# Kernel tuning notes

Hardware: AMD Instinct MI355X
Metric: run time of the kernel (lower is better)

## Reference

```python
import jax, jax.numpy as jnp
import numpy as np

D_MODEL = 1024
N_HEADS = 16
HEAD_DIM = D_MODEL // N_HEADS


def setup_inputs() -> dict:
    key = jax.random.key(0)
    ks = jax.random.split(key, 9)
    B, S = 4, 2048
    x = jax.random.normal(ks[0], (B, S, D_MODEL), dtype=jnp.float32)
    # causal mask, broadcastable to (B, H, S, S); mask==0 -> -inf
    mask = jnp.tril(jnp.ones((S, S), dtype=jnp.int32))[None, None, :, :]
    s = 1.0 / np.sqrt(D_MODEL)
    wq = jax.random.normal(ks[1], (D_MODEL, D_MODEL), dtype=jnp.float32) * s
    wk = jax.random.normal(ks[2], (D_MODEL, D_MODEL), dtype=jnp.float32) * s
    wv = jax.random.normal(ks[3], (D_MODEL, D_MODEL), dtype=jnp.float32) * s
    wo = jax.random.normal(ks[4], (D_MODEL, D_MODEL), dtype=jnp.float32) * s
    bq = jnp.zeros((D_MODEL,), jnp.float32)
    bk = jnp.zeros((D_MODEL,), jnp.float32)
    bv = jnp.zeros((D_MODEL,), jnp.float32)
    bo = jnp.zeros((D_MODEL,), jnp.float32)
    return {"x": x, "mask": mask, "wq": wq, "bq": bq, "wk": wk, "bk": bk,
            "wv": wv, "bv": bv, "wo": wo, "bo": bo}


def reference(x, mask, wq, bq, wk, bk, wv, bv, wo, bo):
    B, S, D = x.shape
    H, Hd = N_HEADS, HEAD_DIM
    # torch nn.Linear: y = x @ W^T + b
    q = (jnp.einsum('bsd,ed->bse', x, wq) + bq).reshape(B, S, H, Hd).transpose(0, 2, 1, 3)
    k = (jnp.einsum('bsd,ed->bse', x, wk) + bk).reshape(B, S, H, Hd).transpose(0, 2, 1, 3)
    v = (jnp.einsum('bsd,ed->bse', x, wv) + bv).reshape(B, S, H, Hd).transpose(0, 2, 1, 3)
    scores = jnp.einsum('bhqd,bhkd->bhqk', q, k) / jnp.sqrt(jnp.float32(Hd))
    scores = jnp.where(mask == 0, -jnp.inf, scores)
    attn = jax.nn.softmax(scores, axis=-1)
    out = jnp.einsum('bhqk,bhkd->bhqd', attn, v)  # (B,H,S,Hd)
    out = out.transpose(0, 2, 1, 3).reshape(B, S, D)
    return jnp.einsum('bsd,ed->bse', out, wo) + bo
```

## Files before the change

kernel.cpp:

```cpp
#include <hip/hip_runtime.h>
#include <hip/hip_bf16.h>
#include <math.h>

using bf16x8 = __attribute__((ext_vector_type(8))) __bf16;
using bf16x4 = __attribute__((ext_vector_type(4))) __bf16;
using f32x4  = __attribute__((ext_vector_type(4))) float;
using f32x16 = __attribute__((ext_vector_type(16))) float;
using u32x4  = __attribute__((ext_vector_type(4))) unsigned;

static constexpr int S_ = 2048;
static constexpr float SCALE_L2E = 0.125f * 1.44269504088896340736f;

__device__ __forceinline__ void gload16(const void* g, void* lds) {
    __builtin_amdgcn_global_load_lds((const __attribute__((address_space(1))) void*)g,
                                     (__attribute__((address_space(3))) void*)lds, 16, 0, 0);
}

__device__ __forceinline__ unsigned pk2(float a, float b) {
    unsigned short lo = __builtin_bit_cast(unsigned short, (__bf16)a);
    unsigned short hi = __builtin_bit_cast(unsigned short, (__bf16)b);
    return (unsigned)lo | ((unsigned)hi << 16);
}

__global__ void cast_f32_bf16(const float* __restrict__ src, __bf16* __restrict__ dst, int n4) {
    int i = blockIdx.x * blockDim.x + threadIdx.x;
    if (i < n4) {
        float4 v = reinterpret_cast<const float4*>(src)[i];
        bf16x4 o = { (__bf16)v.x, (__bf16)v.y, (__bf16)v.z, (__bf16)v.w };
        reinterpret_cast<bf16x4*>(dst)[i] = o;
    }
}

template <int EPI>
__global__ __launch_bounds__(256) void gemm_bt(
    const __bf16* __restrict__ A, const __bf16* __restrict__ Bt,
    const float* __restrict__ b0, const float* __restrict__ b1, const float* __restrict__ b2,
    __bf16* __restrict__ Qo, __bf16* __restrict__ Ko, __bf16* __restrict__ Vo,
    float* __restrict__ Fo, int K) {
    __shared__ __align__(16) __bf16 LDS_[3][2][4096];
    const int t = threadIdx.x, l = t & 63, w = t >> 6;
    const int m0 = blockIdx.y * 128, n0 = blockIdx.x * 128;
    const int wm = (w >> 1) * 64, wn = (w & 1) * 64;
    f32x4 acc[4][4] = {};

    const int row0 = t >> 2, cw0 = t & 3;
    const int gc = cw0 ^ ((row0 >> 1) & 3);
    const __bf16* Ag0 = A + (size_t)(m0 + row0) * K + gc * 8;
    const __bf16* Ag1 = A + (size_t)(m0 + row0 + 64) * K + gc * 8;
    const __bf16* Bg0 = Bt + (size_t)(n0 + row0) * K + gc * 8;
    const __bf16* Bg1 = Bt + (size_t)(n0 + row0 + 64) * K + gc * 8;
    const int wo512 = w * 512;

#define STAGE(buf, k0)                                          \
    do {                                                        \
        gload16(Ag0 + (k0), &LDS_[buf][0][wo512]);              \
        gload16(Ag1 + (k0), &LDS_[buf][0][2048 + wo512]);       \
        gload16(Bg0 + (k0), &LDS_[buf][1][wo512]);              \
        gload16(Bg1 + (k0), &LDS_[buf][1][2048 + wo512]);       \
    } while (0)

    const int nk = K >> 5;
    STAGE(0, 0);
    STAGE(1, 32);
    int rb = 0, sb = 2;
    const int sc = (l >> 4) ^ ((l >> 1) & 3);
    for (int ki = 0; ki < nk; ++ki) {
        if (ki + 2 < nk) {
            STAGE(sb, (ki + 2) << 5);
            asm volatile("s_waitcnt vmcnt(8)" ::: "memory");
        } else if (ki + 1 < nk) {
            asm volatile("s_waitcnt vmcnt(4)" ::: "memory");
        } else {
            asm volatile("s_waitcnt vmcnt(0)" ::: "memory");
        }
        __builtin_amdgcn_s_barrier();
        const char* rdA = (const char*)&LDS_[rb][0][0];
        const char* rdB = (const char*)&LDS_[rb][1][0];
        bf16x8 af[4], bf[4];
#pragma unroll
        for (int i = 0; i < 4; ++i)
            af[i] = *reinterpret_cast<const bf16x8*>(rdA + (wm + i * 16 + (l & 15)) * 64 + sc * 16);
#pragma unroll
        for (int j = 0; j < 4; ++j)
            bf[j] = *reinterpret_cast<const bf16x8*>(rdB + (wn + j * 16 + (l & 15)) * 64 + sc * 16);
#pragma unroll
        for (int i = 0; i < 4; ++i)
#pragma unroll
            for (int j = 0; j < 4; ++j)
                acc[i][j] = __builtin_amdgcn_mfma_f32_16x16x32_bf16(af[i], bf[j], acc[i][j], 0, 0, 0);
        __builtin_amdgcn_s_barrier();
        rb = (rb == 2) ? 0 : rb + 1;
        sb = (sb == 2) ? 0 : sb + 1;
    }
#undef STAGE

    if (EPI == 0) {
        const int cls = n0 >> 10;
        if (cls < 2) {
            const float* bias = (cls == 0) ? b0 : b1;
#pragma unroll
            for (int j = 0; j < 4; ++j) {
                const int e = n0 + wn + j * 16 + (l & 15);
                const int eh = e & 1023;
                const int h = eh >> 6, hd = eh & 63;
                const float bv = bias[eh];
#pragma unroll
                for (int i = 0; i < 4; ++i)
#pragma unroll
                    for (int r = 0; r < 4; ++r) {
                        const int m = m0 + wm + i * 16 + ((l >> 4) << 2) + r;
                        const int b = m >> 11, s = m & 2047;
                        float v = acc[i][j][r] + bv;
                        if (cls == 0) v *= SCALE_L2E;
                        __bf16* dst = (cls == 0) ? Qo : Ko;
                        dst[((size_t)(b * 16 + h) * 2048 + s) * 64 + hd] = (__bf16)v;
                    }
            }
        } else {
            char* Tr = (char*)&LDS_[0][0][0];
#pragma unroll
            for (int j = 0; j < 4; ++j) {
                const int el = wn + j * 16 + (l & 15);
                const float bv = b2[(n0 & 1023) + el];
#pragma unroll
                for (int i = 0; i < 4; ++i) {
                    const int m4 = wm + i * 16 + ((l >> 4) << 2);
                    const int pos0 = (m4 & 112) | ((m4 & 4) << 1) | ((m4 & 8) >> 1);
                    bf16x4 pkv = { (__bf16)(acc[i][j][0] + bv), (__bf16)(acc[i][j][1] + bv),
                                   (__bf16)(acc[i][j][2] + bv), (__bf16)(acc[i][j][3] + bv) };
                    const int byt = el * 256 + ((pos0 * 2) ^ ((el & 7) << 4));
                    *reinterpret_cast<bf16x4*>(Tr + byt) = pkv;
                }
            }
            __syncthreads();
            const int b = m0 >> 11, sblk = m0 & 2047;
#pragma unroll
            for (int rr = 0; rr < 8; ++rr) {
                const int er = w * 32 + rr * 4 + (l >> 4);
                const int c = l & 15;
                const int slot = c ^ (er & 7);
                bf16x8 vv = *reinterpret_cast<const bf16x8*>(Tr + er * 256 + slot * 16);
                const int eg = (n0 & 1023) + er;
                const int h = eg >> 6, hd = eg & 63;
                char* dst = (char*)(Vo + ((size_t)(b * 16 + h) * 64 + hd) * 2048 + sblk) + c * 16;
                *reinterpret_cast<bf16x8*>(dst) = vv;
            }
        }
    } else {
#pragma unroll
        for (int j = 0; j < 4; ++j) {
            const int e = n0 + wn + j * 16 + (l & 15);
            const float bv = b0[e];
#pragma unroll
            for (int i = 0; i < 4; ++i)
#pragma unroll
                for (int r = 0; r < 4; ++r) {
                    const int m = m0 + wm + i * 16 + ((l >> 4) << 2) + r;
                    Fo[(size_t)m * 1024 + e] = acc[i][j][r] + bv;
                }
        }
    }
}

__global__ __launch_bounds__(256, 2) void attn_fwd(
    const __bf16* __restrict__ Qb, const __bf16* __restrict__ Kb,
    const __bf16* __restrict__ VTb, __bf16* __restrict__ Ob) {
    __shared__ __align__(16) __bf16 Ks[2][64 * 64];
    __shared__ __align__(16) __bf16 Vs[2][64 * 64];
    const int t = threadIdx.x, l = t & 63, w = t >> 6;
    const int id = blockIdx.x;
    const int bh = (id & 7) * 8 + ((id >> 3) & 7);
    const int xp = id >> 6;
    const int b = bh >> 4, hh = bh & 15;
    const int hl = l >> 5, l31 = l & 31;

    const __bf16* Qg = Qb + (size_t)bh * S_ * 64;
    const __bf16* Kg = Kb + (size_t)bh * S_ * 64;
    const __bf16* Vg = VTb + (size_t)bh * 64 * S_;

    const int l3 = l >> 3, gc8 = ((l & 7) ^ l3) * 8;
    const __bf16* Ksrc0 = Kg + (size_t)(16 * w + l3) * 64 + gc8;
    const __bf16* Ksrc1 = Kg + (size_t)(16 * w + 8 + l3) * 64 + gc8;
    const __bf16* Vsrc0 = Vg + (size_t)(16 * w + l3) * S_ + gc8;
    const __bf16* Vsrc1 = Vg + (size_t)(16 * w + 8 + l3) * S_ + gc8;
    __bf16* K0a = &Ks[0][w * 1024]; __bf16* K0b = K0a + 512;
    __bf16* K1a = &Ks[1][w * 1024]; __bf16* K1b = K1a + 512;
    __bf16* V0a = &Vs[0][w * 1024]; __bf16* V0b = V0a + 512;
    __bf16* V1a = &Vs[1][w * 1024]; __bf16* V1b = V1a + 512;

#pragma unroll 1
    for (int sidx = 0; sidx < 2; ++sidx) {
        const int qt = (sidx == 0) ? (15 - xp) : xp;
        const int qs = qt * 128 + w * 32;
        const int qg = qs + l31;

        bf16x8 qf[4];
#pragma unroll
        for (int c = 0; c < 4; ++c)
            qf[c] = *reinterpret_cast<const bf16x8*>(Qg + (size_t)qg * 64 + c * 16 + hl * 8);

        f32x16 o0 = {}, o1 = {};
        float m_r = -INFINITY, l_r = 0.f;

        const int ktmax = 2 * qt + 1;
        gload16(Ksrc0, K0a); gload16(Ksrc1, K0b);
        gload16(Vsrc0, V0a); gload16(Vsrc1, V0b);
        int cur = 0;
        for (int kt = 0; kt <= ktmax; ++kt) {
            if (kt < ktmax) {
                const size_t ko = (size_t)(kt + 1) * 4096;
                const int ho = (kt + 1) * 64;
                gload16(Ksrc0 + ko, (cur == 0) ? K1a : K0a);
                gload16(Ksrc1 + ko, (cur == 0) ? K1b : K0b);
                gload16(Vsrc0 + ho, (cur == 0) ? V1a : V0a);
                gload16(Vsrc1 + ho, (cur == 0) ? V1b : V0b);
                asm volatile("s_waitcnt vmcnt(4)" ::: "memory");
            } else {
                asm volatile("s_waitcnt vmcnt(0)" ::: "memory");
            }
            __builtin_amdgcn_s_barrier();
            const char* kb = (cur == 0) ? (const char*)Ks[0] : (const char*)Ks[1];
            const char* vb = (cur == 0) ? (const char*)Vs[0] : (const char*)Vs[1];
            if (kt * 64 <= qs + 31) {
                const int xs = (l & 7) << 4;
                f32x16 s0 = {}, s1 = {};
                __builtin_amdgcn_s_setprio(1);
#pragma unroll
                for (int c = 0; c < 4; ++c) {
                    bf16x8 kf0 = *reinterpret_cast<const bf16x8*>(kb + l31 * 128 + ((c * 32 + hl * 16) ^ xs));
                    s0 = __builtin_amdgcn_mfma_f32_32x32x16_bf16(kf0, qf[c], s0, 0, 0, 0);
                }
#pragma unroll
                for (int c = 0; c < 4; ++c) {
                    bf16x8 kf1 = *reinterpret_cast<const bf16x8*>(kb + (32 + l31) * 128 + ((c * 32 + hl * 16) ^ xs));
                    s1 = __builtin_amdgcn_mfma_f32_32x32x16_bf16(kf1, qf[c], s1, 0, 0, 0);
                }
                __builtin_amdgcn_s_setprio(0);
                float p0[16], p1[16];
                const int ktb = kt * 64;
                const bool bnd = (ktb + 63) > qs;
                if (bnd) {
#pragma unroll
                    for (int r = 0; r < 16; ++r) {
                        const int kvr = ktb + (r & 3) + 8 * (r >> 2) + 4 * hl;
                        p0[r] = (kvr > qg) ? -INFINITY : s0[r];
                        p1[r] = (kvr + 32 > qg) ? -INFINITY : s1[r];
                    }
                } else {
#pragma unroll
                    for (int r = 0; r < 16; ++r) { p0[r] = s0[r]; p1[r] = s1[r]; }
                }
                float mx[16];
#pragma unroll
                for (int r = 0; r < 16; ++r) mx[r] = fmaxf(p0[r], p1[r]);
#pragma unroll
                for (int s2 = 8; s2 > 0; s2 >>= 1)
#pragma unroll
                    for (int r = 0; r < 8; ++r) if (r < s2) mx[r] = fmaxf(mx[r], mx[r + s2]);
                float mt = fmaxf(mx[0], __shfl_xor(mx[0], 32));
                if (!__all(mt - m_r <= 8.0f)) {
                    const float mn = fmaxf(m_r, mt);
                    const float al = exp2f(m_r - mn);
                    m_r = mn;
                    l_r *= al;
#pragma unroll
                    for (int r = 0; r < 16; ++r) { o0[r] *= al; o1[r] *= al; }
                }
                float sm[16];
#pragma unroll
                for (int r = 0; r < 16; ++r) {
                    p0[r] = exp2f(p0[r] - m_r);
                    p1[r] = exp2f(p1[r] - m_r);
                    sm[r] = p0[r] + p1[r];
                }
#pragma unroll
                for (int s2 = 8; s2 > 0; s2 >>= 1)
#pragma unroll
                    for (int r = 0; r < 8; ++r) if (r < s2) sm[r] += sm[r + s2];
                l_r += sm[0] + __shfl_xor(sm[0], 32);
                u32x4 w0 = { pk2(p0[0], p0[1]), pk2(p0[2], p0[3]), pk2(p0[4], p0[5]), pk2(p0[6], p0[7]) };
                u32x4 w1 = { pk2(p0[8], p0[9]), pk2(p0[10], p0[11]), pk2(p0[12], p0[13]), pk2(p0[14], p0[15]) };
                u32x4 w2 = { pk2(p1[0], p1[1]), pk2(p1[2], p1[3]), pk2(p1[4], p1[5]), pk2(p1[6], p1[7]) };
                u32x4 w3 = { pk2(p1[8], p1[9]), pk2(p1[10], p1[11]), pk2(p1[12], p1[13]), pk2(p1[14], p1[15]) };
                bf16x8 pf0 = __builtin_bit_cast(bf16x8, w0);
                bf16x8 pf1 = __builtin_bit_cast(bf16x8, w1);
                bf16x8 pf2 = __builtin_bit_cast(bf16x8, w2);
                bf16x8 pf3 = __builtin_bit_cast(bf16x8, w3);
                __builtin_amdgcn_s_setprio(1);
#pragma unroll
                for (int a = 0; a < 2; ++a) {
                    const int rb2 = (a * 32 + l31) * 128;
                    bf16x8 vf0 = *reinterpret_cast<const bf16x8*>(vb + rb2 + ((0 * 32 + hl * 16) ^ xs));
                    bf16x8 vf1 = *reinterpret_cast<const bf16x8*>(vb + rb2 + ((1 * 32 + hl * 16) ^ xs));
                    bf16x8 vf2 = *reinterpret_cast<const bf16x8*>(vb + rb2 + ((2 * 32 + hl * 16) ^ xs));
                    bf16x8 vf3 = *reinterpret_cast<const bf16x8*>(vb + rb2 + ((3 * 32 + hl * 16) ^ xs));
                    if (a == 0) {
                        o0 = __builtin_amdgcn_mfma_f32_32x32x16_bf16(vf0, pf0, o0, 0, 0, 0);
                        o0 = __builtin_amdgcn_mfma_f32_32x32x16_bf16(vf1, pf1, o0, 0, 0, 0);
                        o0 = __builtin_amdgcn_mfma_f32_32x32x16_bf16(vf2, pf2, o0, 0, 0, 0);
                        o0 = __builtin_amdgcn_mfma_f32_32x32x16_bf16(vf3, pf3, o0, 0, 0, 0);
                    } else {
                        o1 = __builtin_amdgcn_mfma_f32_32x32x16_bf16(vf0, pf0, o1, 0, 0, 0);
                        o1 = __builtin_amdgcn_mfma_f32_32x32x16_bf16(vf1, pf1, o1, 0, 0, 0);
                        o1 = __builtin_amdgcn_mfma_f32_32x32x16_bf16(vf2, pf2, o1, 0, 0, 0);
                        o1 = __builtin_amdgcn_mfma_f32_32x32x16_bf16(vf3, pf3, o1, 0, 0, 0);
                    }
                }
                __builtin_amdgcn_s_setprio(0);
            }
            __builtin_amdgcn_s_barrier();
            cur ^= 1;
        }
        const float inv = 1.0f / l_r;
        __bf16* ob = Ob + (size_t)(b * 2048 + qg) * 1024 + hh * 64;
#pragma unroll
        for (int g = 0; g < 4; ++g) {
            bf16x4 v0 = { (__bf16)(o0[4 * g + 0] * inv), (__bf16)(o0[4 * g + 1] * inv),
                          (__bf16)(o0[4 * g + 2] * inv), (__bf16)(o0[4 * g + 3] * inv) };
            bf16x4 v1 = { (__bf16)(o1[4 * g + 0] * inv), (__bf16)(o1[4 * g + 1] * inv),
                          (__bf16)(o1[4 * g + 2] * inv), (__bf16)(o1[4 * g + 3] * inv) };
            *reinterpret_cast<bf16x4*>(ob + 8 * g + 4 * hl) = v0;
            *reinterpret_cast<bf16x4*>(ob + 32 + 8 * g + 4 * hl) = v1;
        }
    }
}

extern "C" void kernel_launch(void* const* d_in, const int* in_sizes, int n_in,
                              void* d_out, int out_size, void* d_ws, size_t ws_size,
                              hipStream_t stream) {
    const float* x  = (const float*)d_in[0];
    const float* wq = (const float*)d_in[2];
    const float* bq = (const float*)d_in[3];
    const float* wk = (const float*)d_in[4];
    const float* bk = (const float*)d_in[5];
    const float* wv = (const float*)d_in[6];
    const float* bv = (const float*)d_in[7];
    const float* wo = (const float*)d_in[8];
    const float* bo = (const float*)d_in[9];
    float* out = (float*)d_out;

    char* ws = (char*)d_ws;
    __bf16* xb   = (__bf16*)(ws);
    __bf16* wqkv = (__bf16*)(ws + 16777216);
    __bf16* wob  = (__bf16*)(ws + 23068672);
    __bf16* Qb   = (__bf16*)(ws + 25165824);
    __bf16* Kb   = (__bf16*)(ws + 41943040);
    __bf16* VTb  = (__bf16*)(ws + 58720256);
    __bf16* Ob   = (__bf16*)(ws + 75497472);

    cast_f32_bf16<<<8192, 256, 0, stream>>>(x, xb, 2097152);
    cast_f32_bf16<<<1024, 256, 0, stream>>>(wq, wqkv, 262144);
    cast_f32_bf16<<<1024, 256, 0, stream>>>(wk, wqkv + 1048576, 262144);
    cast_f32_bf16<<<1024, 256, 0, stream>>>(wv, wqkv + 2097152, 262144);
    cast_f32_bf16<<<1024, 256, 0, stream>>>(wo, wob, 262144);

    gemm_bt<0><<<dim3(24, 64), 256, 0, stream>>>(xb, wqkv, bq, bk, bv, Qb, Kb, VTb, nullptr, 1024);
    attn_fwd<<<512, 256, 0, stream>>>(Qb, Kb, VTb, Ob);
    gemm_bt<1><<<dim3(8, 64), 256, 0, stream>>>(Ob, wob, bo, nullptr, nullptr, nullptr, nullptr, nullptr, out, 1024);
}
```

Before: 188.0 us.

## Run heavy and light causal query tiles concurrently in one 8-wave block

The attention block now has 512 threads. Four waves handle the long causal query tile and four handle the paired short tile at the same time, instead of one 4-wave block doing the two tiles one after the other. Each K/V tile is loaded from global memory into LDS once and shared by both groups, which halves per-block K/V traffic and removes the serial second pass. The row-max reduction is also rewritten as a tree of 3-input maxes. The cost is that the short-tile waves sit idle at barriers for the rest of the loop. The __launch_bounds__(512,4) hint may also cap registers tightly enough to cause spills.

```diff
diff --git a/kernel.cpp b/kernel.cpp
--- a/kernel.cpp
+++ b/kernel.cpp
@@ -20,6 +20,10 @@
     unsigned short lo = __builtin_bit_cast(unsigned short, (__bf16)a);
     unsigned short hi = __builtin_bit_cast(unsigned short, (__bf16)b);
     return (unsigned)lo | ((unsigned)hi << 16);
+}
+
+__device__ __forceinline__ float max3f(float a, float b, float c) {
+    return fmaxf(fmaxf(a, b), c);
 }
 
 __global__ void cast_f32_bf16(const float* __restrict__ src, __bf16* __restrict__ dst, int n4) {
@@ -162,7 +166,7 @@
     }
 }
 
-__global__ __launch_bounds__(256, 2) void attn_fwd(
+__global__ __launch_bounds__(512, 4) void attn_fwd(
     const __bf16* __restrict__ Qb, const __bf16* __restrict__ Kb,
     const __bf16* __restrict__ VTb, __bf16* __restrict__ Ob) {
     __shared__ __align__(16) __bf16 Ks[2][64 * 64];
@@ -170,7 +174,8 @@
     const int t = threadIdx.x, l = t & 63, w = t >> 6;
     const int id = blockIdx.x;
     const int bh = (id & 7) * 8 + ((id >> 3) & 7);
-    const int xp = id >> 6;
+    const int g = id >> 6;
+    const int xp = (g < 4) ? g : 11 - g;
     const int b = bh >> 4, hh = bh & 15;
     const int hl = l >> 5, l31 = l & 31;
 
@@ -178,150 +183,143 @@
     const __bf16* Kg = Kb + (size_t)bh * S_ * 64;
     const __bf16* Vg = VTb + (size_t)bh * 64 * S_;
 
+    const int qt = (w >> 2) ? xp : (15 - xp);
+    const int sw = w & 3;
+    const int qs = qt * 128 + sw * 32;
+    const int qg = qs + l31;
+
     const int l3 = l >> 3, gc8 = ((l & 7) ^ l3) * 8;
-    const __bf16* Ksrc0 = Kg + (size_t)(16 * w + l3) * 64 + gc8;
-    const __bf16* Ksrc1 = Kg + (size_t)(16 * w + 8 + l3) * 64 + gc8;
-    const __bf16* Vsrc0 = Vg + (size_t)(16 * w + l3) * S_ + gc8;
-    const __bf16* Vsrc1 = Vg + (size_t)(16 * w + 8 + l3) * S_ + gc8;
-    __bf16* K0a = &Ks[0][w * 1024]; __bf16* K0b = K0a + 512;
-    __bf16* K1a = &Ks[1][w * 1024]; __bf16* K1b = K1a + 512;
-    __bf16* V0a = &Vs[0][w * 1024]; __bf16* V0b = V0a + 512;
-    __bf16* V1a = &Vs[1][w * 1024]; __bf16* V1b = V1a + 512;
-
-#pragma unroll 1
-    for (int sidx = 0; sidx < 2; ++sidx) {
-        const int qt = (sidx == 0) ? (15 - xp) : xp;
-        const int qs = qt * 128 + w * 32;
-        const int qg = qs + l31;
-
-        bf16x8 qf[4];
-#pragma unroll
-        for (int c = 0; c < 4; ++c)
-            qf[c] = *reinterpret_cast<const bf16x8*>(Qg + (size_t)qg * 64 + c * 16 + hl * 8);
-
-        f32x16 o0 = {}, o1 = {};
-        float m_r = -INFINITY, l_r = 0.f;
-
-        const int ktmax = 2 * qt + 1;
-        gload16(Ksrc0, K0a); gload16(Ksrc1, K0b);
-        gload16(Vsrc0, V0a); gload16(Vsrc1, V0b);
-        int cur = 0;
-        for (int kt = 0; kt <= ktmax; ++kt) {
-            if (kt < ktmax) {
-                const size_t ko = (size_t)(kt + 1) * 4096;
-                const int ho = (kt + 1) * 64;
-                gload16(Ksrc0 + ko, (cur == 0) ? K1a : K0a);
-                gload16(Ksrc1 + ko, (cur == 0) ? K1b : K0b);
-                gload16(Vsrc0 + ho, (cur == 0) ? V1a : V0a);
-                gload16(Vsrc1 + ho, (cur == 0) ? V1b : V0b);
-                asm volatile("s_waitcnt vmcnt(4)" ::: "memory");
+    const __bf16* Ksrc = Kg + (size_t)(8 * w + l3) * 64 + gc8;
+    const __bf16* Vsrc = Vg + (size_t)(8 * w + l3) * S_ + gc8;
+    __bf16* Kd0 = &Ks[0][w * 512]; __bf16* Kd1 = &Ks[1][w * 512];
+    __bf16* Vd0 = &Vs[0][w * 512]; __bf16* Vd1 = &Vs[1][w * 512];
+
+    bf16x8 qf[4];
+#pragma unroll
+    for (int c = 0; c < 4; ++c)
+        qf[c] = *reinterpret_cast<const bf16x8*>(Qg + (size_t)qg * 64 + c * 16 + hl * 8);
+
+    f32x16 o0 = {}, o1 = {};
+    float m_r = -INFINITY, l_r = 0.f;
+
+    const int ktmax_blk = 2 * (15 - xp) + 1;
+    gload16(Ksrc, Kd0);
+    gload16(Vsrc, Vd0);
+    int cur = 0;
+    for (int kt = 0; kt <= ktmax_blk; ++kt) {
+        if (kt < ktmax_blk) {
+            const size_t ko = (size_t)(kt + 1) * 4096;
+            gload16(Ksrc + ko, (cur == 0) ? Kd1 : Kd0);
+            gload16(Vsrc + (kt + 1) * 64, (cur == 0) ? Vd1 : Vd0);
+            asm volatile("s_waitcnt vmcnt(2)" ::: "memory");
+        } else {
+            asm volatile("s_waitcnt vmcnt(0)" ::: "memory");
+        }
+        __builtin_amdgcn_s_barrier();
+        const char* kb = (cur == 0) ? (const char*)Ks[0] : (const char*)Ks[1];
+        const char* vb = (cur == 0) ? (const char*)Vs[0] : (const char*)Vs[1];
+        if (kt * 64 <= qs + 31) {
+            const int xs = (l & 7) << 4;
+            f32x16 s0 = {}, s1 = {};
+            __builtin_amdgcn_s_setprio(1);
+#pragma unroll
+            for (int c = 0; c < 4; ++c) {
+                bf16x8 kf0 = *reinterpret_cast<const bf16x8*>(kb + l31 * 128 + ((c * 32 + hl * 16) ^ xs));
+                s0 = __builtin_amdgcn_mfma_f32_32x32x16_bf16(kf0, qf[c], s0, 0, 0, 0);
+            }
+#pragma unroll
+            for (int c = 0; c < 4; ++c) {
+                bf16x8 kf1 = *reinterpret_cast<const bf16x8*>(kb + (32 + l31) * 128 + ((c * 32 + hl * 16) ^ xs));
+                s1 = __builtin_amdgcn_mfma_f32_32x32x16_bf16(kf1, qf[c], s1, 0, 0, 0);
+            }
+            __builtin_amdgcn_s_setprio(0);
+            float p0[16], p1[16];
+            const int ktb = kt * 64;
+            const bool bnd = (ktb + 63) > qs;
+            if (bnd) {
+#pragma unroll
+                for (int r = 0; r < 16; ++r) {
+                    const int kvr = ktb + (r & 3) + 8 * (r >> 2) + 4 * hl;
+                    p0[r] = (kvr > qg) ? -INFINITY : s0[r];
+                    p1[r] = (kvr + 32 > qg) ? -INFINITY : s1[r];
+                }
             } else {
-                asm volatile("s_waitcnt vmcnt(0)" ::: "memory");
-            }
-            __builtin_amdgcn_s_barrier();
-            const char* kb = (cur == 0) ? (const char*)Ks[0] : (const char*)Ks[1];
-            const char* vb = (cur == 0) ? (const char*)Vs[0] : (const char*)Vs[1];
-            if (kt * 64 <= qs + 31) {
-                const int xs = (l & 7) << 4;
-                f32x16 s0 = {}, s1 = {};
-                __builtin_amdgcn_s_setprio(1);
-#pragma unroll
-                for (int c = 0; c < 4; ++c) {
-                    bf16x8 kf0 = *reinterpret_cast<const bf16x8*>(kb + l31 * 128 + ((c * 32 + hl * 16) ^ xs));
-                    s0 = __builtin_amdgcn_mfma_f32_32x32x16_bf16(kf0, qf[c], s0, 0, 0, 0);
+#pragma unroll
+                for (int r = 0; r < 16; ++r) { p0[r] = s0[r]; p1[r] = s1[r]; }
+            }
+            float mx[16];
+#pragma unroll
+            for (int r = 0; r < 16; ++r) mx[r] = fmaxf(p0[r], p1[r]);
+            float u0 = max3f(mx[0], mx[1], mx[2]);
+            float u1 = max3f(mx[3], mx[4], mx[5]);
+            float u2 = max3f(mx[6], mx[7], mx[8]);
+            float u3 = max3f(mx[9], mx[10], mx[11]);
+            float u4 = max3f(mx[12], mx[13], mx[14]);
+            float mt = fmaxf(max3f(u0, u1, u2), max3f(u3, u4, mx[15]));
+            mt = fmaxf(mt, __shfl_xor(mt, 32));
+            if (!__all(mt - m_r <= 8.0f)) {
+                const float mn = fmaxf(m_r, mt);
+                const float al = exp2f(m_r - mn);
+                m_r = mn;
+                l_r *= al;
+#pragma unroll
+                for (int r = 0; r < 16; ++r) { o0[r] *= al; o1[r] *= al; }
+            }
+            float sm[16];
+#pragma unroll
+            for (int r = 0; r < 16; ++r) {
+                p0[r] = exp2f(p0[r] - m_r);
+                p1[r] = exp2f(p1[r] - m_r);
+                sm[r] = p0[r] + p1[r];
+            }
+#pragma unroll
+            for (int s2 = 8; s2 > 0; s2 >>= 1)
+#pragma unroll
+                for (int r = 0; r < 8; ++r) if (r < s2) sm[r] += sm[r + s2];
+            l_r += sm[0] + __shfl_xor(sm[0], 32);
+            u32x4 w0 = { pk2(p0[0], p0[1]), pk2(p0[2], p0[3]), pk2(p0[4], p0[5]), pk2(p0[6], p0[7]) };
+            u32x4 w1 = { pk2(p0[8], p0[9]), pk2(p0[10], p0[11]), pk2(p0[12], p0[13]), pk2(p0[14], p0[15]) };
+            u32x4 w2 = { pk2(p1[0], p1[1]), pk2(p1[2], p1[3]), pk2(p1[4], p1[5]), pk2(p1[6], p1[7]) };
+            u32x4 w3 = { pk2(p1[8], p1[9]), pk2(p1[10], p1[11]), pk2(p1[12], p1[13]), pk2(p1[14], p1[15]) };
+            bf16x8 pf0 = __builtin_bit_cast(bf16x8, w0);
+            bf16x8 pf1 = __builtin_bit_cast(bf16x8, w1);
+            bf16x8 pf2 = __builtin_bit_cast(bf16x8, w2);
+            bf16x8 pf3 = __builtin_bit_cast(bf16x8, w3);
+            __builtin_amdgcn_s_setprio(1);
+#pragma unroll
+            for (int a = 0; a < 2; ++a) {
+                const int rb2 = (a * 32 + l31) * 128;
+                bf16x8 vf0 = *reinterpret_cast<const bf16x8*>(vb + rb2 + ((0 * 32 + hl * 16) ^ xs));
+                bf16x8 vf1 = *reinterpret_cast<const bf16x8*>(vb + rb2 + ((1 * 32 + hl * 16) ^ xs));
+                bf16x8 vf2 = *reinterpret_cast<const bf16x8*>(vb + rb2 + ((2 * 32 + hl * 16) ^ xs));
+                bf16x8 vf3 = *reinterpret_cast<const bf16x8*>(vb + rb2 + ((3 * 32 + hl * 16) ^ xs));
+                if (a == 0) {
+                    o0 = __builtin_amdgcn_mfma_f32_32x32x16_bf16(vf0, pf0, o0, 0, 0, 0);
+                    o0 = __builtin_amdgcn_mfma_f32_32x32x16_bf16(vf1, pf1, o0, 0, 0, 0);
+                    o0 = __builtin_amdgcn_mfma_f32_32x32x16_bf16(vf2, pf2, o0, 0, 0, 0);
+                    o0 = __builtin_amdgcn_mfma_f32_32x32x16_bf16(vf3, pf3, o0, 0, 0, 0);
+                } else {
+                    o1 = __builtin_amdgcn_mfma_f32_32x32x16_bf16(vf0, pf0, o1, 0, 0, 0);
+                    o1 = __builtin_amdgcn_mfma_f32_32x32x16_bf16(vf1, pf1, o1, 0, 0, 0);
+                    o1 = __builtin_amdgcn_mfma_f32_32x32x16_bf16(vf2, pf2, o1, 0, 0, 0);
+                    o1 = __builtin_amdgcn_mfma_f32_32x32x16_bf16(vf3, pf3, o1, 0, 0, 0);
                 }
-#pragma unroll
-                for (int c = 0; c < 4; ++c) {
-                    bf16x8 kf1 = *reinterpret_cast<const bf16x8*>(kb + (32 + l31) * 128 + ((c * 32 + hl * 16) ^ xs));
-                    s1 = __builtin_amdgcn_mfma_f32_32x32x16_bf16(kf1, qf[c], s1, 0, 0, 0);
-                }
-                __builtin_amdgcn_s_setprio(0);
-                float p0[16], p1[16];
-                const int ktb = kt * 64;
-                const bool bnd = (ktb + 63) > qs;
-                if (bnd) {
-#pragma unroll
-                    for (int r = 0; r < 16; ++r) {
-                        const int kvr = ktb + (r & 3) + 8 * (r >> 2) + 4 * hl;
-                        p0[r] = (kvr > qg) ? -INFINITY : s0[r];
-                        p1[r] = (kvr + 32 > qg) ? -INFINITY : s1[r];
-                    }
-                } else {
-#pragma unroll
-                    for (int r = 0; r < 16; ++r) { p0[r] = s0[r]; p1[r] = s1[r]; }
-                }
-                float mx[16];
-#pragma unroll
-                for (int r = 0; r < 16; ++r) mx[r] = fmaxf(p0[r], p1[r]);
-#pragma unroll
-                for (int s2 = 8; s2 > 0; s2 >>= 1)
-#pragma unroll
-                    for (int r = 0; r < 8; ++r) if (r < s2) mx[r] = fmaxf(mx[r], mx[r + s2]);
-                float mt = fmaxf(mx[0], __shfl_xor(mx[0], 32));
-                if (!__all(mt - m_r <= 8.0f)) {
-                    const float mn = fmaxf(m_r, mt);
-                    const float al = exp2f(m_r - mn);
-                    m_r = mn;
-                    l_r *= al;
-#pragma unroll
-                    for (int r = 0; r < 16; ++r) { o0[r] *= al; o1[r] *= al; }
-                }
-                float sm[16];
-#pragma unroll
-                for (int r = 0; r < 16; ++r) {
-                    p0[r] = exp2f(p0[r] - m_r);
-                    p1[r] = exp2f(p1[r] - m_r);
-                    sm[r] = p0[r] + p1[r];
-                }
-#pragma unroll
-                for (int s2 = 8; s2 > 0; s2 >>= 1)
-#pragma unroll
-                    for (int r = 0; r < 8; ++r) if (r < s2) sm[r] += sm[r + s2];
-                l_r += sm[0] + __shfl_xor(sm[0], 32);
-                u32x4 w0 = { pk2(p0[0], p0[1]), pk2(p0[2], p0[3]), pk2(p0[4], p0[5]), pk2(p0[6], p0[7]) };
-                u32x4 w1 = { pk2(p0[8], p0[9]), pk2(p0[10], p0[11]), pk2(p0[12], p0[13]), pk2(p0[14], p0[15]) };
-                u32x4 w2 = { pk2(p1[0], p1[1]), pk2(p1[2], p1[3]), pk2(p1[4], p1[5]), pk2(p1[6], p1[7]) };
-                u32x4 w3 = { pk2(p1[8], p1[9]), pk2(p1[10], p1[11]), pk2(p1[12], p1[13]), pk2(p1[14], p1[15]) };
-                bf16x8 pf0 = __builtin_bit_cast(bf16x8, w0);
-                bf16x8 pf1 = __builtin_bit_cast(bf16x8, w1);
-                bf16x8 pf2 = __builtin_bit_cast(bf16x8, w2);
-                bf16x8 pf3 = __builtin_bit_cast(bf16x8, w3);
-                __builtin_amdgcn_s_setprio(1);
-#pragma unroll
-                for (int a = 0; a < 2; ++a) {
-                    const int rb2 = (a * 32 + l31) * 128;
-                    bf16x8 vf0 = *reinterpret_cast<const bf16x8*>(vb + rb2 + ((0 * 32 + hl * 16) ^ xs));
-                    bf16x8 vf1 = *reinterpret_cast<const bf16x8*>(vb + rb2 + ((1 * 32 + hl * 16) ^ xs));
-                    bf16x8 vf2 = *reinterpret_cast<const bf16x8*>(vb + rb2 + ((2 * 32 + hl * 16) ^ xs));
-                    bf16x8 vf3 = *reinterpret_cast<const bf16x8*>(vb + rb2 + ((3 * 32 + hl * 16) ^ xs));
-                    if (a == 0) {
-                        o0 = __builtin_amdgcn_mfma_f32_32x32x16_bf16(vf0, pf0, o0, 0, 0, 0);
-                        o0 = __builtin_amdgcn_mfma_f32_32x32x16_bf16(vf1, pf1, o0, 0, 0, 0);
-                        o0 = __builtin_amdgcn_mfma_f32_32x32x16_bf16(vf2, pf2, o0, 0, 0, 0);
-                        o0 = __builtin_amdgcn_mfma_f32_32x32x16_bf16(vf3, pf3, o0, 0, 0, 0);
-                    } else {
-                        o1 = __builtin_amdgcn_mfma_f32_32x32x16_bf16(vf0, pf0, o1, 0, 0, 0);
-                        o1 = __builtin_amdgcn_mfma_f32_32x32x16_bf16(vf1, pf1, o1, 0, 0, 0);
-                        o1 = __builtin_amdgcn_mfma_f32_32x32x16_bf16(vf2, pf2, o1, 0, 0, 0);
-                        o1 = __builtin_amdgcn_mfma_f32_32x32x16_bf16(vf3, pf3, o1, 0, 0, 0);
-                    }
-                }
-                __builtin_amdgcn_s_setprio(0);
-            }
-            __builtin_amdgcn_s_barrier();
-            cur ^= 1;
-        }
-        const float inv = 1.0f / l_r;
-        __bf16* ob = Ob + (size_t)(b * 2048 + qg) * 1024 + hh * 64;
-#pragma unroll
-        for (int g = 0; g < 4; ++g) {
-            bf16x4 v0 = { (__bf16)(o0[4 * g + 0] * inv), (__bf16)(o0[4 * g + 1] * inv),
-                          (__bf16)(o0[4 * g + 2] * inv), (__bf16)(o0[4 * g + 3] * inv) };
-            bf16x4 v1 = { (__bf16)(o1[4 * g + 0] * inv), (__bf16)(o1[4 * g + 1] * inv),
-                          (__bf16)(o1[4 * g + 2] * inv), (__bf16)(o1[4 * g + 3] * inv) };
-            *reinterpret_cast<bf16x4*>(ob + 8 * g + 4 * hl) = v0;
-            *reinterpret_cast<bf16x4*>(ob + 32 + 8 * g + 4 * hl) = v1;
-        }
+            }
+            __builtin_amdgcn_s_setprio(0);
+        }
+        __builtin_amdgcn_s_barrier();
+        cur ^= 1;
+    }
+    const float inv = 1.0f / l_r;
+    __bf16* ob = Ob + (size_t)(b * 2048 + qg) * 1024 + hh * 64;
+#pragma unroll
+    for (int gq = 0; gq < 4; ++gq) {
+        bf16x4 v0 = { (__bf16)(o0[4 * gq + 0] * inv), (__bf16)(o0[4 * gq + 1] * inv),
+                      (__bf16)(o0[4 * gq + 2] * inv), (__bf16)(o0[4 * gq + 3] * inv) };
+        bf16x4 v1 = { (__bf16)(o1[4 * gq + 0] * inv), (__bf16)(o1[4 * gq + 1] * inv),
+                      (__bf16)(o1[4 * gq + 2] * inv), (__bf16)(o1[4 * gq + 3] * inv) };
+        *reinterpret_cast<bf16x4*>(ob + 8 * gq + 4 * hl) = v0;
+        *reinterpret_cast<bf16x4*>(ob + 32 + 8 * gq + 4 * hl) = v1;
     }
 }
 
@@ -355,6 +353,6 @@
     cast_f32_bf16<<<1024, 256, 0, stream>>>(wo, wob, 262144);
 
     gemm_bt<0><<<dim3(24, 64), 256, 0, stream>>>(xb, wqkv, bq, bk, bv, Qb, Kb, VTb, nullptr, 1024);
-    attn_fwd<<<512, 256, 0, stream>>>(Qb, Kb, VTb, Ob);
+    attn_fwd<<<512, 512, 0, stream>>>(Qb, Kb, VTb, Ob);
     gemm_bt<1><<<dim3(8, 64), 256, 0, stream>>>(Ob, wob, bo, nullptr, nullptr, nullptr, nullptr, nullptr, out, 1024);
 }
```

Result: no change. 185.0 us (-1.6%).
